# Kernel optimization log

Hardware: AMD Instinct MI355X
Metric: run time of the kernel (lower is better)

The kernel has to match this reference:

```python
import jax, jax.numpy as jnp
import numpy as np

N_NODES = 100000
N_EDGES = 1600000
IN_FEATS = 128
N_HIDDEN = 32
N_CLASSES = 47
HEADS = (4, 4)
NEG_SLOPE = 0.2


def setup_inputs() -> dict:
    key = jax.random.key(0)
    ks = jax.random.split(key, 12)
    x = jax.random.normal(ks[0], (N_NODES, IN_FEATS), dtype=jnp.float32)
    src = jax.random.randint(ks[1], (N_EDGES,), 0, N_NODES)
    dst = jax.random.randint(ks[2], (N_EDGES,), 0, N_NODES)
    inverse_idx = jax.random.randint(ks[3], (N_NODES,), 0, N_NODES)
    h1 = HEADS[0] * N_HIDDEN
    s1 = 1.0 / np.sqrt(IN_FEATS)
    W1 = jax.random.normal(ks[4], (IN_FEATS, h1), dtype=jnp.float32) * s1
    al1 = jax.random.normal(ks[5], (HEADS[0], N_HIDDEN), dtype=jnp.float32) * 0.1
    ar1 = jax.random.normal(ks[6], (HEADS[0], N_HIDDEN), dtype=jnp.float32) * 0.1
    b1 = jnp.zeros((h1,), dtype=jnp.float32)
    h2 = HEADS[1] * N_CLASSES
    s2 = 1.0 / np.sqrt(h1)
    W2 = jax.random.normal(ks[7], (h1, h2), dtype=jnp.float32) * s2
    al2 = jax.random.normal(ks[8], (HEADS[1], N_CLASSES), dtype=jnp.float32) * 0.1
    ar2 = jax.random.normal(ks[9], (HEADS[1], N_CLASSES), dtype=jnp.float32) * 0.1
    b2 = jnp.zeros((h2,), dtype=jnp.float32)
    return {"x": x, "src": src, "dst": dst, "inverse_idx": inverse_idx,
            "W1": W1, "al1": al1, "ar1": ar1, "b1": b1,
            "W2": W2, "al2": al2, "ar2": ar2, "b2": b2}


def gat_conv(h, src, dst, W, al, ar, b, heads, out_dim, apply_elu):
    # DGL GATConv (feat_drop=attn_drop=0, eval mode):
    # projected per-head features, edge attention, per-dst softmax, aggregate.
    feat = (h @ W).reshape(-1, heads, out_dim)               # (N, H, D)
    el = jnp.einsum('nhd,hd->nh', feat, al)                  # (N, H)
    er = jnp.einsum('nhd,hd->nh', feat, ar)                  # (N, H)
    e = el[src] + er[dst]                                    # (E, H)
    e = jnp.where(e > 0, e, NEG_SLOPE * e)                   # LeakyReLU
    m = jax.ops.segment_max(e, dst, num_segments=N_NODES)    # (N, H)
    m = jnp.where(jnp.isfinite(m), m, 0.0)
    ex = jnp.exp(e - m[dst])
    s = jax.ops.segment_sum(ex, dst, num_segments=N_NODES)   # (N, H)
    alpha = ex / jnp.maximum(s[dst], 1e-9)                   # (E, H)
    msg = feat[src] * alpha[:, :, None]                      # (E, H, D)
    out = jax.ops.segment_sum(msg, dst, num_segments=N_NODES)  # (N, H, D)
    out = out + b.reshape(1, heads, out_dim)
    if apply_elu:
        out = jax.nn.elu(out)
    return out


def reference(x, src, dst, inverse_idx, W1, al1, ar1, b1, W2, al2, ar2, b2):
    # Layer 0: GATConv + ELU, flatten heads, then NPFeatureShuffle reindex.
    h = gat_conv(x, src, dst, W1, al1, ar1, b1, HEADS[0], N_HIDDEN, True)
    h = h.reshape(N_NODES, HEADS[0] * N_HIDDEN)
    h = h[inverse_idx]  # cross-partition shuffle reindex
    # Layer 1: GATConv, no activation, mean over heads.
    h = gat_conv(h, src, dst, W2, al2, ar2, b2, HEADS[1], N_CLASSES, False)
    return h.mean(axis=1)  # (N, n_classes)
```

## Files before the change

kernel.cpp:

```cpp
#include <hip/hip_runtime.h>
#include <hip/hip_bf16.h>
#include <hip/hip_fp16.h>
#include <type_traits>

#define N_NODES 100000
#define N_EDGES 1600000

typedef _Float16 half8_t __attribute__((ext_vector_type(8)));
typedef _Float16 half4_t __attribute__((ext_vector_type(4)));
typedef float floatx4 __attribute__((ext_vector_type(4)));

__global__ void count_deg(const int* __restrict__ dst, int* __restrict__ deg, int E) {
    int i = blockIdx.x * blockDim.x + threadIdx.x;
    if (i < E) atomicAdd(&deg[dst[i]], 1);
}

__global__ void block_sums(const int* __restrict__ deg, int* __restrict__ bsum, int N) {
    __shared__ int ws[4];
    const int t = threadIdx.x;
    int i = blockIdx.x * 256 + t;
    int v = (i < N) ? deg[i] : 0;
    #pragma unroll
    for (int o = 32; o; o >>= 1) v += __shfl_down(v, o, 64);
    if ((t & 63) == 0) ws[t >> 6] = v;
    __syncthreads();
    if (t == 0) bsum[blockIdx.x] = ws[0] + ws[1] + ws[2] + ws[3];
}

__global__ void scan_bsum(int* __restrict__ bsum, int nb) {
    __shared__ int sh[512];
    const int t = threadIdx.x;
    sh[t] = (t < nb) ? bsum[t] : 0;
    __syncthreads();
    for (int o = 1; o < 512; o <<= 1) {
        int v = (t >= o) ? sh[t - o] : 0;
        __syncthreads();
        sh[t] += v;
        __syncthreads();
    }
    if (t < nb) bsum[t] = sh[t];
}

__global__ void scan_final(const int* __restrict__ deg, const int* __restrict__ bsum,
                           int* __restrict__ row_ptr, int* __restrict__ cursor, int N) {
    __shared__ int ws[4];
    const int t = threadIdx.x;
    const int b = blockIdx.x;
    const int i = b * 256 + t;
    const int lane = t & 63;
    const int wid = t >> 6;
    int v = (i < N) ? deg[i] : 0;
    int x = v;
    #pragma unroll
    for (int o = 1; o < 64; o <<= 1) {
        int y = __shfl_up(x, o, 64);
        if (lane >= o) x += y;
    }
    if (lane == 63) ws[wid] = x;
    __syncthreads();
    int prefix = (b > 0) ? bsum[b - 1] : 0;
    for (int k = 0; k < wid; ++k) prefix += ws[k];
    if (i < N) {
        row_ptr[i + 1] = prefix + x;
        cursor[i] = prefix + x - v;
    }
    if (i == 0) row_ptr[0] = 0;
}

__global__ void scatter_edges_part(const int* __restrict__ src, const int* __restrict__ dst,
                                   int* __restrict__ cursor, int* __restrict__ e_src, int E) {
    const int part = blockIdx.x & 7;
    const int sb = blockIdx.x >> 3;
    const int nslices = gridDim.x >> 3;
    const int psz = N_NODES / 8;
    const int lo = part * psz;
    const int hi = (part == 7) ? N_NODES : lo + psz;
    const int begin = (int)((long long)E * sb / nslices);
    const int end = (int)((long long)E * (sb + 1) / nslices);
    for (int i = begin + threadIdx.x; i < end; i += blockDim.x) {
        int d = dst[i];
        if (d >= lo && d < hi) {
            int p = atomicAdd(&cursor[d], 1);
            e_src[p] = src[i];
        }
    }
}

__global__ void prep_w(const float* __restrict__ W1, const float* __restrict__ W2,
                       const float* __restrict__ al1, const float* __restrict__ ar1,
                       const float* __restrict__ al2, const float* __restrict__ ar2,
                       __half* __restrict__ Wt1, __half* __restrict__ Wt2) {
    const int c = blockIdx.x;
    const int k = threadIdx.x;
    if (c < 128) {
        Wt1[c * 128 + k] = __float2half(W1[k * 128 + c]);
    } else if (c < 144) {
        int j = c - 128;
        float v = 0.f;
        if (j < 8) {
            int h = j & 3;
            const float* a = (j < 4) ? al1 : ar1;
            for (int d = 0; d < 32; ++d)
                v = fmaf(W1[k * 128 + h * 32 + d], a[h * 32 + d], v);
        }
        Wt1[c * 128 + k] = __float2half(v);
    } else if (c < 336) {
        int c2 = c - 144;
        float v = (c2 < 188) ? W2[k * 188 + c2] : 0.f;
        Wt2[c2 * 128 + k] = __float2half(v);
    } else {
        int j = c - 336;
        float v = 0.f;
        if (j < 8) {
            int h = j & 3;
            const float* a = (j < 4) ? al2 : ar2;
            for (int d = 0; d < 47; ++d)
                v = fmaf(W2[k * 188 + h * 47 + d], a[h * 47 + d], v);
        }
        Wt2[(192 + j) * 128 + k] = __float2half(v);
    }
}

template <int TT, int NLOG, int OSTRIDE, bool PADSTORE, bool GATHER, typename AT>
__global__ __launch_bounds__(256) void gemm_mfma(
    const AT* __restrict__ A, const __half* __restrict__ Wt,
    __half* __restrict__ C, float* __restrict__ el, float* __restrict__ er,
    const int* __restrict__ gather, int N) {
    constexpr int LDA = 136;
    __shared__ _Float16 As[64 * LDA];
    __shared__ int ridx[64];
    const int tid = threadIdx.x;
    const int r0 = blockIdx.x * 64;

    if (tid < 64) {
        int row = r0 + tid;
        int pr = 0;
        if (row < N) pr = GATHER ? gather[row] : row;
        ridx[tid] = pr;
    }
    __syncthreads();

    {
        const int r = tid >> 2, q = tid & 3;
        const int src = ridx[r];
        if constexpr (std::is_same<AT, float>::value) {
            const float4* A4 = (const float4*)A;
            #pragma unroll
            for (int i = 0; i < 8; ++i) {
                float4 v = A4[(size_t)src * 32 + q * 8 + i];
                half4_t hv = {(_Float16)v.x, (_Float16)v.y, (_Float16)v.z, (_Float16)v.w};
                *(half4_t*)&As[r * LDA + q * 32 + i * 4] = hv;
            }
        } else {
            const uint4* A4 = (const uint4*)A;
            #pragma unroll
            for (int i = 0; i < 4; ++i) {
                uint4 v = A4[(size_t)src * 16 + q * 4 + i];
                *(uint4*)&As[r * LDA + q * 32 + i * 8] = v;
            }
        }
    }
    __syncthreads();

    const int lane = tid & 63;
    const int wave = tid >> 6;
    const int col = lane & 15;
    const int quad = lane >> 4;
    const int arow = wave * 16 + col;

    floatx4 acc[TT];
    #pragma unroll
    for (int t = 0; t < TT; ++t) acc[t] = (floatx4){0.f, 0.f, 0.f, 0.f};

    #pragma unroll
    for (int kc = 0; kc < 4; ++kc) {
        half8_t a = *(const half8_t*)&As[arow * LDA + kc * 32 + quad * 8];
        #pragma unroll
        for (int t = 0; t < TT; ++t) {
            half8_t b = *(const half8_t*)&Wt[(size_t)(t * 16 + col) * 128 + kc * 32 + quad * 8];
            acc[t] = __builtin_amdgcn_mfma_f32_16x16x32_f16(a, b, acc[t], 0, 0, 0);
        }
    }

    #pragma unroll
    for (int t = 0; t < TT - 1; ++t) {
        #pragma unroll
        for (int r = 0; r < 4; ++r) {
            int row = r0 + wave * 16 + quad * 4 + r;
            int c = t * 16 + col;
            if (row < N && c < NLOG) {
                int sc = PADSTORE ? (c + c / 47) : c;
                C[(size_t)row * OSTRIDE + sc] = __float2half(acc[t][r]);
            }
        }
    }
    #pragma unroll
    for (int r = 0; r < 4; ++r) {
        int row = r0 + wave * 16 + quad * 4 + r;
        if (row < N) {
            if (col < 4) el[row * 4 + col] = acc[TT - 1][r];
            else if (col < 8) er[row * 4 + (col - 4)] = acc[TT - 1][r];
        }
    }
}

__global__ __launch_bounds__(256) void gat_gather1(
    const __half* __restrict__ feat, const float* __restrict__ el,
    const float* __restrict__ er,
    const int* __restrict__ row_ptr, const int* __restrict__ e_src,
    const float* __restrict__ bias, __half* __restrict__ out) {
    const int t = threadIdx.x;
    const int lane = t & 63;
    const int n = blockIdx.x * 4 + (t >> 6);
    const int h = lane >> 4;
    const int start = row_ptr[n], end = row_ptr[n + 1];
    const __half2* f2 = (const __half2*)feat;
    const float ern = er[n * 4 + h];
    float ax = 0.f, ay = 0.f, s = 0.f;
    int i = start;
    for (; i + 4 <= end; i += 4) {
        int sv0 = e_src[i + 0], sv1 = e_src[i + 1], sv2 = e_src[i + 2], sv3 = e_src[i + 3];
        float e0 = el[sv0 * 4 + h] + ern;
        float e1 = el[sv1 * 4 + h] + ern;
        float e2 = el[sv2 * 4 + h] + ern;
        float e3 = el[sv3 * 4 + h] + ern;
        float w0 = __expf(fmaxf(e0, 0.2f * e0));
        float w1 = __expf(fmaxf(e1, 0.2f * e1));
        float w2 = __expf(fmaxf(e2, 0.2f * e2));
        float w3 = __expf(fmaxf(e3, 0.2f * e3));
        __half2 f0 = f2[(size_t)sv0 * 64 + lane];
        __half2 f1 = f2[(size_t)sv1 * 64 + lane];
        __half2 f2v = f2[(size_t)sv2 * 64 + lane];
        __half2 f3 = f2[(size_t)sv3 * 64 + lane];
        float2 g0 = __half22float2(f0), g1 = __half22float2(f1);
        float2 g2 = __half22float2(f2v), g3 = __half22float2(f3);
        s += (w0 + w1) + (w2 + w3);
        ax += w0 * g0.x + w1 * g1.x + w2 * g2.x + w3 * g3.x;
        ay += w0 * g0.y + w1 * g1.y + w2 * g2.y + w3 * g3.y;
    }
    for (; i < end; ++i) {
        int sv = e_src[i];
        float e = el[sv * 4 + h] + ern;
        float ww = __expf(fmaxf(e, 0.2f * e));
        float2 g = __half22float2(f2[(size_t)sv * 64 + lane]);
        s += ww;
        ax += ww * g.x;
        ay += ww * g.y;
    }
    float inv = 1.f / fmaxf(s, 1e-9f);
    float ox = ax * inv + bias[lane * 2 + 0];
    float oy = ay * inv + bias[lane * 2 + 1];
    ox = (ox > 0.f) ? ox : (__expf(ox) - 1.f);
    oy = (oy > 0.f) ? oy : (__expf(oy) - 1.f);
    ((__half2*)out)[(size_t)n * 64 + lane] = __floats2half2_rn(ox, oy);
}

__global__ __launch_bounds__(256) void gat_gather2(
    const __half* __restrict__ feat, const float* __restrict__ el,
    const float* __restrict__ er,
    const int* __restrict__ row_ptr, const int* __restrict__ e_src,
    const float* __restrict__ bias, float* __restrict__ out) {
    const int t = threadIdx.x;
    const int lane = t & 63;
    const int n = blockIdx.x * 4 + (t >> 6);
    if (lane < 48) {
        const int h = lane / 12;
        const int q = lane - h * 12;
        const int start = row_ptr[n], end = row_ptr[n + 1];
        const half4_t* f4 = (const half4_t*)feat;
        const float ern = er[n * 4 + h];
        float a0 = 0.f, a1 = 0.f, a2 = 0.f, a3 = 0.f, s = 0.f;
        int i = start;
        for (; i + 4 <= end; i += 4) {
            int sv0 = e_src[i + 0], sv1 = e_src[i + 1], sv2 = e_src[i + 2], sv3 = e_src[i + 3];
            float e0 = el[sv0 * 4 + h] + ern;
            float e1 = el[sv1 * 4 + h] + ern;
            float e2 = el[sv2 * 4 + h] + ern;
            float e3 = el[sv3 * 4 + h] + ern;
            float w0 = __expf(fmaxf(e0, 0.2f * e0));
            float w1 = __expf(fmaxf(e1, 0.2f * e1));
            float w2 = __expf(fmaxf(e2, 0.2f * e2));
            float w3 = __expf(fmaxf(e3, 0.2f * e3));
            half4_t f0 = f4[(size_t)sv0 * 48 + lane];
            half4_t f1 = f4[(size_t)sv1 * 48 + lane];
            half4_t f2 = f4[(size_t)sv2 * 48 + lane];
            half4_t f3 = f4[(size_t)sv3 * 48 + lane];
            s += (w0 + w1) + (w2 + w3);
            a0 += w0 * (float)f0[0] + w1 * (float)f1[0] + w2 * (float)f2[0] + w3 * (float)f3[0];
            a1 += w0 * (float)f0[1] + w1 * (float)f1[1] + w2 * (float)f2[1] + w3 * (float)f3[1];
            a2 += w0 * (float)f0[2] + w1 * (float)f1[2] + w2 * (float)f2[2] + w3 * (float)f3[2];
            a3 += w0 * (float)f0[3] + w1 * (float)f1[3] + w2 * (float)f2[3] + w3 * (float)f3[3];
        }
        for (; i < end; ++i) {
            int sv = e_src[i];
            float e = el[sv * 4 + h] + ern;
            float ww = __expf(fmaxf(e, 0.2f * e));
            half4_t f0 = f4[(size_t)sv * 48 + lane];
            s += ww;
            a0 += ww * (float)f0[0];
            a1 += ww * (float)f0[1];
            a2 += ww * (float)f0[2];
            a3 += ww * (float)f0[3];
        }
        if (q == 11) a3 = 0.f;
        float inv = 1.f / fmaxf(s, 1e-9f);
        const int d0 = q * 4;
        float b0 = bias[h * 47 + d0 + 0];
        float b1 = bias[h * 47 + d0 + 1];
        float b2 = bias[h * 47 + d0 + 2];
        float b3 = (d0 + 3 < 47) ? bias[h * 47 + d0 + 3] : 0.f;
        float r0 = a0 * inv + b0;
        float r1 = a1 * inv + b1;
        float r2 = a2 * inv + b2;
        float r3 = a3 * inv + b3;
        float t0 = r0 + __shfl(r0, lane + 12, 64) + __shfl(r0, lane + 24, 64) + __shfl(r0, lane + 36, 64);
        float t1 = r1 + __shfl(r1, lane + 12, 64) + __shfl(r1, lane + 24, 64) + __shfl(r1, lane + 36, 64);
        float t2 = r2 + __shfl(r2, lane + 12, 64) + __shfl(r2, lane + 24, 64) + __shfl(r2, lane + 36, 64);
        float t3 = r3 + __shfl(r3, lane + 12, 64) + __shfl(r3, lane + 24, 64) + __shfl(r3, lane + 36, 64);
        if (h == 0) {
            size_t base = (size_t)n * 47 + d0;
            out[base + 0] = 0.25f * t0;
            out[base + 1] = 0.25f * t1;
            out[base + 2] = 0.25f * t2;
            if (d0 + 3 < 47) out[base + 3] = 0.25f * t3;
        }
    }
}

extern "C" void kernel_launch(void* const* d_in, const int* in_sizes, int n_in,
                              void* d_out, int out_size, void* d_ws, size_t ws_size,
                              hipStream_t stream) {
    const int N = N_NODES, E = N_EDGES;
    const float* x    = (const float*)d_in[0];
    const int*   src  = (const int*)d_in[1];
    const int*   dst  = (const int*)d_in[2];
    const int*   inv  = (const int*)d_in[3];
    const float* W1   = (const float*)d_in[4];
    const float* al1  = (const float*)d_in[5];
    const float* ar1  = (const float*)d_in[6];
    const float* b1   = (const float*)d_in[7];
    const float* W2   = (const float*)d_in[8];
    const float* al2  = (const float*)d_in[9];
    const float* ar2  = (const float*)d_in[10];
    const float* b2   = (const float*)d_in[11];
    float* out = (float*)d_out;

    char* p = (char*)d_ws;
    auto carve = [&](size_t bytes) {
        char* q = p;
        p += (bytes + 255) & ~size_t(255);
        return q;
    };
    __half* feat1   = (__half*)carve((size_t)N * 128 * 2);
    __half* feat2   = (__half*)carve((size_t)N * 192 * 2);
    __half* hbuf    = (__half*)carve((size_t)N * 128 * 2);
    __half* Wt1     = (__half*)carve(144 * 128 * 2);
    __half* Wt2     = (__half*)carve(208 * 128 * 2);
    float*  el      = (float*)carve((size_t)N * 4 * 4);
    float*  er      = (float*)carve((size_t)N * 4 * 4);
    int*    deg     = (int*)carve((size_t)N * 4);
    int*    row_ptr = (int*)carve((size_t)(N + 1) * 4);
    int*    cursor  = (int*)carve((size_t)N * 4);
    int*    bsum    = (int*)carve(512 * 4);
    int*    e_src   = (int*)carve((size_t)E * 4);

    const int nb = (N + 255) / 256;

    hipMemsetAsync(deg, 0, (size_t)N * 4, stream);
    count_deg<<<(E + 255) / 256, 256, 0, stream>>>(dst, deg, E);
    block_sums<<<nb, 256, 0, stream>>>(deg, bsum, N);
    scan_bsum<<<1, 512, 0, stream>>>(bsum, nb);
    scan_final<<<nb, 256, 0, stream>>>(deg, bsum, row_ptr, cursor, N);
    scatter_edges_part<<<2048, 256, 0, stream>>>(src, dst, cursor, e_src, E);

    prep_w<<<352, 128, 0, stream>>>(W1, W2, al1, ar1, al2, ar2, Wt1, Wt2);

    gemm_mfma<9, 128, 128, false, false, float><<<(N + 63) / 64, 256, 0, stream>>>(
        x, Wt1, feat1, el, er, nullptr, N);
    gat_gather1<<<(N + 3) / 4, 256, 0, stream>>>(feat1, el, er, row_ptr, e_src, b1, hbuf);

    gemm_mfma<13, 188, 192, true, true, __half><<<(N + 63) / 64, 256, 0, stream>>>(
        hbuf, Wt2, feat2, el, er, inv, N);
    gat_gather2<<<(N + 3) / 4, 256, 0, stream>>>(feat2, el, er, row_ptr, e_src, b2, out);
}
```

Measured before the change: 532.4 us.

## Embed layer-2 el into feature padding, store layer-1 el as fp16, fuse prep kernels

```diff
diff --git a/kernel.cpp b/kernel.cpp
--- a/kernel.cpp
+++ b/kernel.cpp
@@ -10,9 +10,47 @@
 typedef _Float16 half4_t __attribute__((ext_vector_type(4)));
 typedef float floatx4 __attribute__((ext_vector_type(4)));
 
-__global__ void count_deg(const int* __restrict__ dst, int* __restrict__ deg, int E) {
-    int i = blockIdx.x * blockDim.x + threadIdx.x;
-    if (i < E) atomicAdd(&deg[dst[i]], 1);
+__global__ void csr_prep(const int* __restrict__ dst, int* __restrict__ deg, int E,
+                         const float* __restrict__ W1, const float* __restrict__ W2,
+                         const float* __restrict__ al1, const float* __restrict__ ar1,
+                         const float* __restrict__ al2, const float* __restrict__ ar2,
+                         __half* __restrict__ Wt1, __half* __restrict__ Wt2) {
+    const int b = blockIdx.x;
+    if (b < 6250) {
+        int i = b * 256 + threadIdx.x;
+        if (i < E) atomicAdd(&deg[dst[i]], 1);
+        return;
+    }
+    const int c = b - 6250;
+    const int k = threadIdx.x;
+    if (k >= 128) return;
+    if (c < 128) {
+        Wt1[c * 128 + k] = __float2half(W1[k * 128 + c]);
+    } else if (c < 144) {
+        int j = c - 128;
+        float v = 0.f;
+        if (j < 8) {
+            int h = j & 3;
+            const float* a = (j < 4) ? al1 : ar1;
+            for (int d = 0; d < 32; ++d)
+                v = fmaf(W1[k * 128 + h * 32 + d], a[h * 32 + d], v);
+        }
+        Wt1[c * 128 + k] = __float2half(v);
+    } else if (c < 336) {
+        int c2 = c - 144;
+        float v = (c2 < 188) ? W2[k * 188 + c2] : 0.f;
+        Wt2[c2 * 128 + k] = __float2half(v);
+    } else {
+        int j = c - 336;
+        float v = 0.f;
+        if (j < 8) {
+            int h = j & 3;
+            const float* a = (j < 4) ? al2 : ar2;
+            for (int d = 0; d < 47; ++d)
+                v = fmaf(W2[k * 188 + h * 47 + d], a[h * 47 + d], v);
+        }
+        Wt2[(192 + j) * 128 + k] = __float2half(v);
+    }
 }
 
 __global__ void block_sums(const int* __restrict__ deg, int* __restrict__ bsum, int N) {
@@ -86,45 +124,10 @@
     }
 }
 
-__global__ void prep_w(const float* __restrict__ W1, const float* __restrict__ W2,
-                       const float* __restrict__ al1, const float* __restrict__ ar1,
-                       const float* __restrict__ al2, const float* __restrict__ ar2,
-                       __half* __restrict__ Wt1, __half* __restrict__ Wt2) {
-    const int c = blockIdx.x;
-    const int k = threadIdx.x;
-    if (c < 128) {
-        Wt1[c * 128 + k] = __float2half(W1[k * 128 + c]);
-    } else if (c < 144) {
-        int j = c - 128;
-        float v = 0.f;
-        if (j < 8) {
-            int h = j & 3;
-            const float* a = (j < 4) ? al1 : ar1;
-            for (int d = 0; d < 32; ++d)
-                v = fmaf(W1[k * 128 + h * 32 + d], a[h * 32 + d], v);
-        }
-        Wt1[c * 128 + k] = __float2half(v);
-    } else if (c < 336) {
-        int c2 = c - 144;
-        float v = (c2 < 188) ? W2[k * 188 + c2] : 0.f;
-        Wt2[c2 * 128 + k] = __float2half(v);
-    } else {
-        int j = c - 336;
-        float v = 0.f;
-        if (j < 8) {
-            int h = j & 3;
-            const float* a = (j < 4) ? al2 : ar2;
-            for (int d = 0; d < 47; ++d)
-                v = fmaf(W2[k * 188 + h * 47 + d], a[h * 47 + d], v);
-        }
-        Wt2[(192 + j) * 128 + k] = __float2half(v);
-    }
-}
-
-template <int TT, int NLOG, int OSTRIDE, bool PADSTORE, bool GATHER, typename AT>
+template <int TT, int NLOG, int OSTRIDE, bool EMBED, bool GATHER, typename AT>
 __global__ __launch_bounds__(256) void gemm_mfma(
     const AT* __restrict__ A, const __half* __restrict__ Wt,
-    __half* __restrict__ C, float* __restrict__ el, float* __restrict__ er,
+    __half* __restrict__ C, __half* __restrict__ elh, float* __restrict__ er,
     const int* __restrict__ gather, int N) {
     constexpr int LDA = 136;
     __shared__ _Float16 As[64 * LDA];
@@ -189,7 +192,7 @@
             int row = r0 + wave * 16 + quad * 4 + r;
             int c = t * 16 + col;
             if (row < N && c < NLOG) {
-                int sc = PADSTORE ? (c + c / 47) : c;
+                int sc = EMBED ? (c + c / 47) : c;
                 C[(size_t)row * OSTRIDE + sc] = __float2half(acc[t][r]);
             }
         }
@@ -198,14 +201,20 @@
     for (int r = 0; r < 4; ++r) {
         int row = r0 + wave * 16 + quad * 4 + r;
         if (row < N) {
-            if (col < 4) el[row * 4 + col] = acc[TT - 1][r];
-            else if (col < 8) er[row * 4 + (col - 4)] = acc[TT - 1][r];
+            if (col < 4) {
+                if constexpr (EMBED)
+                    C[(size_t)row * OSTRIDE + col * 48 + 47] = __float2half(acc[TT - 1][r]);
+                else
+                    elh[row * 4 + col] = __float2half(acc[TT - 1][r]);
+            } else if (col < 8) {
+                er[row * 4 + (col - 4)] = acc[TT - 1][r];
+            }
         }
     }
 }
 
 __global__ __launch_bounds__(256) void gat_gather1(
-    const __half* __restrict__ feat, const float* __restrict__ el,
+    const __half* __restrict__ feat, const __half* __restrict__ elh,
     const float* __restrict__ er,
     const int* __restrict__ row_ptr, const int* __restrict__ e_src,
     const float* __restrict__ bias, __half* __restrict__ out) {
@@ -220,10 +229,10 @@
     int i = start;
     for (; i + 4 <= end; i += 4) {
         int sv0 = e_src[i + 0], sv1 = e_src[i + 1], sv2 = e_src[i + 2], sv3 = e_src[i + 3];
-        float e0 = el[sv0 * 4 + h] + ern;
-        float e1 = el[sv1 * 4 + h] + ern;
-        float e2 = el[sv2 * 4 + h] + ern;
-        float e3 = el[sv3 * 4 + h] + ern;
+        float e0 = __half2float(elh[sv0 * 4 + h]) + ern;
+        float e1 = __half2float(elh[sv1 * 4 + h]) + ern;
+        float e2 = __half2float(elh[sv2 * 4 + h]) + ern;
+        float e3 = __half2float(elh[sv3 * 4 + h]) + ern;
         float w0 = __expf(fmaxf(e0, 0.2f * e0));
         float w1 = __expf(fmaxf(e1, 0.2f * e1));
         float w2 = __expf(fmaxf(e2, 0.2f * e2));
@@ -240,7 +249,7 @@
     }
     for (; i < end; ++i) {
         int sv = e_src[i];
-        float e = el[sv * 4 + h] + ern;
+        float e = __half2float(elh[sv * 4 + h]) + ern;
         float ww = __expf(fmaxf(e, 0.2f * e));
         float2 g = __half22float2(f2[(size_t)sv * 64 + lane]);
         s += ww;
@@ -256,8 +265,7 @@
 }
 
 __global__ __launch_bounds__(256) void gat_gather2(
-    const __half* __restrict__ feat, const float* __restrict__ el,
-    const float* __restrict__ er,
+    const __half* __restrict__ feat, const float* __restrict__ er,
     const int* __restrict__ row_ptr, const int* __restrict__ e_src,
     const float* __restrict__ bias, float* __restrict__ out) {
     const int t = threadIdx.x;
@@ -266,6 +274,7 @@
     if (lane < 48) {
         const int h = lane / 12;
         const int q = lane - h * 12;
+        const int g11 = h * 12 + 11;
         const int start = row_ptr[n], end = row_ptr[n + 1];
         const half4_t* f4 = (const half4_t*)feat;
         const float ern = er[n * 4 + h];
@@ -273,18 +282,18 @@
         int i = start;
         for (; i + 4 <= end; i += 4) {
             int sv0 = e_src[i + 0], sv1 = e_src[i + 1], sv2 = e_src[i + 2], sv3 = e_src[i + 3];
-            float e0 = el[sv0 * 4 + h] + ern;
-            float e1 = el[sv1 * 4 + h] + ern;
-            float e2 = el[sv2 * 4 + h] + ern;
-            float e3 = el[sv3 * 4 + h] + ern;
+            half4_t f0 = f4[(size_t)sv0 * 48 + lane];
+            half4_t f1 = f4[(size_t)sv1 * 48 + lane];
+            half4_t f2 = f4[(size_t)sv2 * 48 + lane];
+            half4_t f3 = f4[(size_t)sv3 * 48 + lane];
+            float e0 = __shfl((float)f0[3], g11, 64) + ern;
+            float e1 = __shfl((float)f1[3], g11, 64) + ern;
+            float e2 = __shfl((float)f2[3], g11, 64) + ern;
+            float e3 = __shfl((float)f3[3], g11, 64) + ern;
             float w0 = __expf(fmaxf(e0, 0.2f * e0));
             float w1 = __expf(fmaxf(e1, 0.2f * e1));
             float w2 = __expf(fmaxf(e2, 0.2f * e2));
             float w3 = __expf(fmaxf(e3, 0.2f * e3));
-            half4_t f0 = f4[(size_t)sv0 * 48 + lane];
-            half4_t f1 = f4[(size_t)sv1 * 48 + lane];
-            half4_t f2 = f4[(size_t)sv2 * 48 + lane];
-            half4_t f3 = f4[(size_t)sv3 * 48 + lane];
             s += (w0 + w1) + (w2 + w3);
             a0 += w0 * (float)f0[0] + w1 * (float)f1[0] + w2 * (float)f2[0] + w3 * (float)f3[0];
             a1 += w0 * (float)f0[1] + w1 * (float)f1[1] + w2 * (float)f2[1] + w3 * (float)f3[1];
@@ -293,9 +302,9 @@
         }
         for (; i < end; ++i) {
             int sv = e_src[i];
-            float e = el[sv * 4 + h] + ern;
+            half4_t f0 = f4[(size_t)sv * 48 + lane];
+            float e = __shfl((float)f0[3], g11, 64) + ern;
             float ww = __expf(fmaxf(e, 0.2f * e));
-            half4_t f0 = f4[(size_t)sv * 48 + lane];
             s += ww;
             a0 += ww * (float)f0[0];
             a1 += ww * (float)f0[1];
@@ -356,7 +365,7 @@
     __half* hbuf    = (__half*)carve((size_t)N * 128 * 2);
     __half* Wt1     = (__half*)carve(144 * 128 * 2);
     __half* Wt2     = (__half*)carve(208 * 128 * 2);
-    float*  el      = (float*)carve((size_t)N * 4 * 4);
+    __half* elh1    = (__half*)carve((size_t)N * 4 * 2);
     float*  er      = (float*)carve((size_t)N * 4 * 4);
     int*    deg     = (int*)carve((size_t)N * 4);
     int*    row_ptr = (int*)carve((size_t)(N + 1) * 4);
@@ -367,19 +376,17 @@
     const int nb = (N + 255) / 256;
 
     hipMemsetAsync(deg, 0, (size_t)N * 4, stream);
-    count_deg<<<(E + 255) / 256, 256, 0, stream>>>(dst, deg, E);
+    csr_prep<<<6250 + 352, 256, 0, stream>>>(dst, deg, E, W1, W2, al1, ar1, al2, ar2, Wt1, Wt2);
     block_sums<<<nb, 256, 0, stream>>>(deg, bsum, N);
     scan_bsum<<<1, 512, 0, stream>>>(bsum, nb);
     scan_final<<<nb, 256, 0, stream>>>(deg, bsum, row_ptr, cursor, N);
     scatter_edges_part<<<2048, 256, 0, stream>>>(src, dst, cursor, e_src, E);
 
-    prep_w<<<352, 128, 0, stream>>>(W1, W2, al1, ar1, al2, ar2, Wt1, Wt2);
-
     gemm_mfma<9, 128, 128, false, false, float><<<(N + 63) / 64, 256, 0, stream>>>(
-        x, Wt1, feat1, el, er, nullptr, N);
-    gat_gather1<<<(N + 3) / 4, 256, 0, stream>>>(feat1, el, er, row_ptr, e_src, b1, hbuf);
+        x, Wt1, feat1, elh1, er, nullptr, N);
+    gat_gather1<<<(N + 3) / 4, 256, 0, stream>>>(feat1, elh1, er, row_ptr, e_src, b1, hbuf);
 
     gemm_mfma<13, 188, 192, true, true, __half><<<(N + 63) / 64, 256, 0, stream>>>(
-        hbuf, Wt2, feat2, el, er, inv, N);
-    gat_gather2<<<(N + 3) / 4, 256, 0, stream>>>(feat2, el, er, row_ptr, e_src, b2, out);
-}
+        hbuf, Wt2, feat2, nullptr, er, inv, N);
+    gat_gather2<<<(N + 3) / 4, 256, 0, stream>>>(feat2, er, row_ptr, e_src, b2, out);
+}
```

Result: faster. 521.1 us (-2.1%).
